# Optimization experiments

Hardware: AMD Instinct MI355X
Metric: run time of the kernel (lower is better)

Reference implementation:

```python
import jax, jax.numpy as jnp
import numpy as np

B, LQ, LK, E, H = 8, 1024, 1024, 512, 8
D = E // H
NEG = -2.0**32 + 1  # padding value used by original torch code


def setup_inputs() -> dict:
    key = jax.random.key(0)
    ks = jax.random.split(key, 6)
    s = 0.02
    return {
        "x1": jax.random.normal(ks[0], (B, LQ, E), jnp.float32),
        "x2": jax.random.normal(ks[1], (B, LK, E), jnp.float32),
        "Wq": jax.random.normal(ks[2], (E, E), jnp.float32) * s,
        "bq": jnp.zeros((E,), jnp.float32),
        "Wk": jax.random.normal(ks[3], (E, E), jnp.float32) * s,
        "bk": jnp.zeros((E,), jnp.float32),
        "Wv": jax.random.normal(ks[4], (E, E), jnp.float32) * s,
        "bv": jnp.zeros((E,), jnp.float32),
    }


def _split_heads(t):
    # torch: cat(split(t, E//H, dim=2), dim=0) -> head-major [H, B, L, D]
    b, l, _ = t.shape
    return jnp.moveaxis(t.reshape(b, l, H, D), 2, 0)


def reference(x1, x2, Wq, bq, Wk, bk, Wv, bv):
    # ReLU-activated projections (nn.Linear: x @ W.T + b)
    q = jax.nn.relu(x1 @ Wq.T + bq)  # [B,LQ,E]
    k = jax.nn.relu(x2 @ Wk.T + bk)  # [B,LK,E]
    v = jax.nn.relu(x2 @ Wv.T + bv)  # [B,LK,E]

    q_, k_, v_ = _split_heads(q), _split_heads(k), _split_heads(v)  # [H,B,L,D]

    # scaled scores; original scales by sqrt(emb_size), not sqrt(d_head)
    scores = jnp.einsum('hbqd,hbkd->hbqk', q_, k_) / jnp.sqrt(jnp.float32(E))

    # sin-based key mask from raw x2
    key_mask = jnp.sin(jnp.abs(jnp.sum(x2, -1)))  # [B,LK]
    scores = jnp.where(key_mask[None, :, None, :] <= 0, NEG, scores)

    attn = jax.nn.softmax(scores, axis=-1)

    # sin-based query mask from raw x1, applied after softmax
    query_mask = jnp.sin(jnp.abs(jnp.sum(x1, -1)))  # [B,LQ]
    attn = attn * query_mask[None, :, :, None]

    out = jnp.einsum('hbqk,hbkd->hbqd', attn, v_)  # [H,B,LQ,D]
    out = jnp.moveaxis(out, 0, 2).reshape(B, LQ, E)  # merge heads back
    return out + q  # residual add with activated query projection
```

## Files before the change

kernel.cpp:

```cpp
#include <hip/hip_runtime.h>
#include <hip/hip_bf16.h>
#include <math.h>

typedef short bf16x8 __attribute__((ext_vector_type(8)));
typedef float f32x4 __attribute__((ext_vector_type(4)));
typedef unsigned int u32;
typedef unsigned short u16;

constexpr int Bb = 8, LQn = 1024, LKn = 1024, En = 512, Hn = 8, Dn = 64;
constexpr int Mtok = Bb * LQn;
constexpr float KCOEF = 0.06376246332977306f;

__device__ __forceinline__ u16 f2bf(float f) {
  u32 u = __builtin_bit_cast(u32, f);
  u32 r = (u + 0x7fffu + ((u >> 16) & 1u)) >> 16;
  return (u16)r;
}
__device__ __forceinline__ float bf2f(u16 h) {
  u32 u = ((u32)h) << 16;
  return __builtin_bit_cast(float, u);
}
__device__ __forceinline__ u16 f2bf_hw(float f) {
  return __builtin_bit_cast(u16, __float2bfloat16(f));
}

__device__ __forceinline__ void async_lds16(const void* gsrc, void* ldst) {
  __builtin_amdgcn_global_load_lds(
      (const __attribute__((address_space(1))) u32*)gsrc,
      (__attribute__((address_space(3))) u32*)ldst, 16, 0, 0);
}

__global__ void prep_kernel(const float* __restrict__ x1, const float* __restrict__ x2,
                            u16* __restrict__ x1b, u16* __restrict__ x2b,
                            float* __restrict__ qmask, float* __restrict__ kbias,
                            const float* __restrict__ Wq, const float* __restrict__ Wk,
                            const float* __restrict__ Wv, u16* __restrict__ wqb,
                            u16* __restrict__ wkb, u16* __restrict__ wvb) {
  int blk = blockIdx.x;
  if (blk < 4096) {
    int id = blk * 4 + (threadIdx.x >> 6);
    int lane = threadIdx.x & 63;
    const float* x; u16* xb; int row; bool isq;
    if (id < Mtok) { x = x1; xb = x1b; row = id; isq = true; }
    else           { x = x2; xb = x2b; row = id - Mtok; isq = false; }
    const float4* p = reinterpret_cast<const float4*>(x + (size_t)row * En);
    ushort4* ob = reinterpret_cast<ushort4*>(xb + (size_t)row * En);
    double s = 0.0;
#pragma unroll
    for (int j = 0; j < En / 256; ++j) {
      float4 v = p[lane + j * 64];
      s += (double)v.x + (double)v.y + (double)v.z + (double)v.w;
      ushort4 o;
      o.x = f2bf(v.x); o.y = f2bf(v.y); o.z = f2bf(v.z); o.w = f2bf(v.w);
      ob[lane + j * 64] = o;
    }
#pragma unroll
    for (int off = 32; off > 0; off >>= 1) s += __shfl_down(s, off, 64);
    if (lane == 0) {
      float sv = (float)sin(fabs(s));
      if (isq) qmask[row] = sv;
      else     kbias[row] = sv > 0.f ? 0.f : -3.0e38f;
    }
  } else {
    int n4 = En * En / 4;
    int j = (blk - 4096) * 256 + threadIdx.x;
    const float* src; u16* dst;
    if (j < n4) { src = Wq; dst = wqb; }
    else if (j < 2 * n4) { src = Wk; dst = wkb; j -= n4; }
    else { src = Wv; dst = wvb; j -= 2 * n4; }
    float4 v = reinterpret_cast<const float4*>(src)[j];
    ushort4 o;
    o.x = f2bf(v.x); o.y = f2bf(v.y); o.z = f2bf(v.z); o.w = f2bf(v.w);
    reinterpret_cast<ushort4*>(dst)[j] = o;
  }
}

template <int BIAS_ROW>
__device__ __forceinline__ void gemm_core(
    const u16* __restrict__ A, const u16* __restrict__ Bm,
    const float* __restrict__ bias, u16* __restrict__ C,
    int ldc, float coef, int row0, int col0) {
  constexpr int K = 512, BK = 64;
  __shared__ u16 sA[2][128 * BK];
  __shared__ u16 sB[2][128 * BK];
  int tid = threadIdx.x;
  int lane = tid & 63;
  int w = tid >> 6;
  int wm = w >> 2, wn = w & 3;
  int rgrp = lane >> 4, cidx = lane & 15;

  f32x4 acc[4][2];
#pragma unroll
  for (int mi = 0; mi < 4; ++mi)
#pragma unroll
    for (int ni = 0; ni < 2; ++ni) acc[mi][ni] = f32x4{0.f, 0.f, 0.f, 0.f};

  auto stage = [&](int kt, int buf) {
    int k0 = kt * BK;
#pragma unroll
    for (int rr = 0; rr < 2; ++rr) {
      int cid = rr * 512 + tid;
      int r = cid >> 3, c = cid & 7;
      int cg = c ^ (r & 7);
      async_lds16(A + (size_t)(row0 + r) * K + k0 + cg * 8, &sA[buf][cid * 8]);
    }
#pragma unroll
    for (int rr = 0; rr < 2; ++rr) {
      int cid = rr * 512 + tid;
      int r = cid >> 3, c = cid & 7;
      int cg = c ^ (r & 7);
      async_lds16(Bm + (size_t)(col0 + r) * K + k0 + cg * 8, &sB[buf][cid * 8]);
    }
  };

  stage(0, 0);
  __syncthreads();

  for (int kt = 0; kt < K / BK; ++kt) {
    int cur = kt & 1;
    if (kt < K / BK - 1) stage(kt + 1, cur ^ 1);
#pragma unroll
    for (int kk = 0; kk < 2; ++kk) {
      bf16x8 a[4], b[2];
#pragma unroll
      for (int mi = 0; mi < 4; ++mi) {
        int row = wm * 64 + mi * 16 + cidx;
        a[mi] = *reinterpret_cast<const bf16x8*>(
            &sA[cur][row * BK + ((kk * 4 + rgrp) ^ (row & 7)) * 8]);
      }
#pragma unroll
      for (int ni = 0; ni < 2; ++ni) {
        int row = wn * 32 + ni * 16 + cidx;
        b[ni] = *reinterpret_cast<const bf16x8*>(
            &sB[cur][row * BK + ((kk * 4 + rgrp) ^ (row & 7)) * 8]);
      }
#pragma unroll
      for (int mi = 0; mi < 4; ++mi)
#pragma unroll
        for (int ni = 0; ni < 2; ++ni)
          acc[mi][ni] = __builtin_amdgcn_mfma_f32_16x16x32_bf16(a[mi], b[ni], acc[mi][ni], 0, 0, 0);
    }
    __syncthreads();
  }
#pragma unroll
  for (int mi = 0; mi < 4; ++mi)
#pragma unroll
    for (int ni = 0; ni < 2; ++ni)
#pragma unroll
      for (int r = 0; r < 4; ++r) {
        int grow = row0 + wm * 64 + mi * 16 + rgrp * 4 + r;
        int gcol = col0 + wn * 32 + ni * 16 + cidx;
        float v = acc[mi][ni][r] + (BIAS_ROW ? bias[grow] : bias[gcol]);
        v = v > 0.f ? v : 0.f;
        C[(size_t)grow * ldc + gcol] = f2bf(v * coef);
      }
}

__global__ __launch_bounds__(512, 4) void gemm3(
    const u16* __restrict__ x1b, const u16* __restrict__ wqb, const float* __restrict__ bq,
    u16* __restrict__ qbq,
    const u16* __restrict__ x2b, const u16* __restrict__ wkb, const float* __restrict__ bk,
    u16* __restrict__ kbk,
    const u16* __restrict__ wvb, const float* __restrict__ bv, u16* __restrict__ vtb) {
  int z = blockIdx.z;
  if (z == 0) {
    gemm_core<0>(x1b, wqb, bq, qbq, En, 1.0f, blockIdx.x * 128, blockIdx.y * 128);
  } else if (z == 1) {
    gemm_core<0>(x2b, wkb, bk, kbk, En, KCOEF, blockIdx.x * 128, blockIdx.y * 128);
  } else {
    gemm_core<1>(wvb, x2b, bv, vtb, Mtok, 1.0f, blockIdx.y * 128, blockIdx.x * 128);
  }
}

__global__ __launch_bounds__(256, 4) void attn_kernel(
    const u16* __restrict__ qb, const u16* __restrict__ kb, const u16* __restrict__ vtb,
    const float* __restrict__ kbias, const float* __restrict__ qmask,
    float* __restrict__ out) {
  __shared__ u16 sK[2][64 * 64];
  __shared__ u16 sV[2][64 * 64];
  __shared__ u16 sQP[64 * 64];
  int tid = threadIdx.x, lane = tid & 63, w = tid >> 6;
  int bh = blockIdx.x, qblk = blockIdx.y;
  int b = bh >> 3, h = bh & 7;
  int rgrp = lane >> 4, cidx = lane & 15;

  const u16* qbase = qb + ((size_t)(b * LQn) + qblk * 64) * En + h * Dn;
  const u16* kbase = kb + (size_t)(b * LKn) * En + h * Dn;
  const u16* vbase = vtb + (size_t)(h * Dn) * Mtok + b * LKn;
  const float* kmb = kbias + b * LKn;

  auto stageKV = [&](int kt, int buf) {
#pragma unroll
    for (int rr = 0; rr < 2; ++rr) {
      int cid = rr * 256 + tid;
      int r = cid >> 3, c = cid & 7;
      int cg = c ^ (r & 7);
      async_lds16(kbase + (size_t)(kt * 64 + r) * En + cg * 8, &sK[buf][cid * 8]);
      async_lds16(vbase + (size_t)r * Mtok + kt * 64 + cg * 8, &sV[buf][cid * 8]);
    }
  };

#pragma unroll
  for (int rr = 0; rr < 2; ++rr) {
    int cid = rr * 256 + tid;
    int r = cid >> 3, c = cid & 7;
    int cg = c ^ (r & 7);
    async_lds16(qbase + (size_t)r * En + cg * 8, &sQP[cid * 8]);
  }
  stageKV(0, 0);
  __syncthreads();

  bf16x8 qa0, qa1;
  {
    int row = w * 16 + cidx;
    qa0 = *reinterpret_cast<const bf16x8*>(&sQP[row * 64 + (rgrp ^ (row & 7)) * 8]);
    qa1 = *reinterpret_cast<const bf16x8*>(&sQP[row * 64 + ((4 + rgrp) ^ (row & 7)) * 8]);
  }

  f32x4 acc_o[4];
#pragma unroll
  for (int dt = 0; dt < 4; ++dt) acc_o[dt] = f32x4{0.f, 0.f, 0.f, 0.f};
  float den = 0.f;

  int prow = w * 16 + cidx;
  char* sPbyte = reinterpret_cast<char*>(sQP);

  for (int kt = 0; kt < LKn / 64; ++kt) {
    int cur = kt & 1;
    if (kt < LKn / 64 - 1) stageKV(kt + 1, cur ^ 1);
#pragma unroll
    for (int ktile = 0; ktile < 4; ++ktile) {
      int krow = ktile * 16 + cidx;
      bf16x8 kf0 = *reinterpret_cast<const bf16x8*>(
          &sK[cur][krow * 64 + (rgrp ^ (krow & 7)) * 8]);
      bf16x8 kf1 = *reinterpret_cast<const bf16x8*>(
          &sK[cur][krow * 64 + ((4 + rgrp) ^ (krow & 7)) * 8]);
      float4 km4 = *reinterpret_cast<const float4*>(&kmb[kt * 64 + ktile * 16 + rgrp * 4]);
      f32x4 s;
      s[0] = km4.x; s[1] = km4.y; s[2] = km4.z; s[3] = km4.w;
      s = __builtin_amdgcn_mfma_f32_16x16x32_bf16(kf0, qa0, s, 0, 0, 0);
      s = __builtin_amdgcn_mfma_f32_16x16x32_bf16(kf1, qa1, s, 0, 0, 0);
      float p0 = __builtin_amdgcn_exp2f(s[0]);
      float p1 = __builtin_amdgcn_exp2f(s[1]);
      float p2 = __builtin_amdgcn_exp2f(s[2]);
      float p3 = __builtin_amdgcn_exp2f(s[3]);
      den += (p0 + p1) + (p2 + p3);
      ushort4 pk;
      pk.x = f2bf_hw(p0); pk.y = f2bf_hw(p1); pk.z = f2bf_hw(p2); pk.w = f2bf_hw(p3);
      int gran = ktile * 2 + (rgrp >> 1);
      int boff = prow * 128 + ((gran ^ (prow & 7)) << 4) + ((rgrp & 1) << 3);
      *reinterpret_cast<ushort4*>(sPbyte + boff) = pk;
    }
    __builtin_amdgcn_s_setprio(1);
#pragma unroll
    for (int kk = 0; kk < 2; ++kk) {
      bf16x8 pa = *reinterpret_cast<const bf16x8*>(
          &sQP[prow * 64 + ((kk * 4 + rgrp) ^ (prow & 7)) * 8]);
#pragma unroll
      for (int dt = 0; dt < 4; ++dt) {
        int vrow = dt * 16 + cidx;
        bf16x8 vf = *reinterpret_cast<const bf16x8*>(
            &sV[cur][vrow * 64 + ((kk * 4 + rgrp) ^ (vrow & 7)) * 8]);
        acc_o[dt] = __builtin_amdgcn_mfma_f32_16x16x32_bf16(pa, vf, acc_o[dt], 0, 0, 0);
      }
    }
    __builtin_amdgcn_s_setprio(0);
    __syncthreads();
  }
  den += __shfl_xor(den, 16, 64);
  den += __shfl_xor(den, 32, 64);

  const float* qmb = qmask + (size_t)b * LQn + qblk * 64 + w * 16;
  const u16* qres = qbase + (size_t)(w * 16) * En;
  float* obase = out + ((size_t)(b * LQn) + qblk * 64 + w * 16) * En + h * Dn;
#pragma unroll
  for (int r = 0; r < 4; ++r) {
    int qr = rgrp * 4 + r;
    float denq = __shfl(den, qr, 64);
    float fac = qmb[qr] / denq;
#pragma unroll
    for (int dt = 0; dt < 4; ++dt) {
      float v = acc_o[dt][r] * fac + bf2f(qres[(size_t)qr * En + dt * 16 + cidx]);
      obase[(size_t)qr * En + dt * 16 + cidx] = v;
    }
  }
}

extern "C" void kernel_launch(void* const* d_in, const int* in_sizes, int n_in,
                              void* d_out, int out_size, void* d_ws, size_t ws_size,
                              hipStream_t stream) {
  const float* x1 = (const float*)d_in[0];
  const float* x2 = (const float*)d_in[1];
  const float* Wq = (const float*)d_in[2];
  const float* bq = (const float*)d_in[3];
  const float* Wk = (const float*)d_in[4];
  const float* bk = (const float*)d_in[5];
  const float* Wv = (const float*)d_in[6];
  const float* bv = (const float*)d_in[7];
  float* out = (float*)d_out;

  char* ws = (char*)d_ws;
  size_t o = 0;
  u16* x1b = (u16*)(ws + o); o += (size_t)Mtok * En * 2;
  u16* x2b = (u16*)(ws + o); o += (size_t)Mtok * En * 2;
  u16* wqb = (u16*)(ws + o); o += (size_t)En * En * 2;
  u16* wkb = (u16*)(ws + o); o += (size_t)En * En * 2;
  u16* wvb = (u16*)(ws + o); o += (size_t)En * En * 2;
  u16* qbq = (u16*)(ws + o); o += (size_t)Mtok * En * 2;
  u16* kbk = (u16*)(ws + o); o += (size_t)Mtok * En * 2;
  u16* vtb = (u16*)(ws + o); o += (size_t)Mtok * En * 2;
  float* kbias = (float*)(ws + o); o += (size_t)Mtok * 4;
  float* qmask = (float*)(ws + o); o += (size_t)Mtok * 4;

  prep_kernel<<<4864, 256, 0, stream>>>(x1, x2, x1b, x2b, qmask, kbias,
                                        Wq, Wk, Wv, wqb, wkb, wvb);

  dim3 g3(Mtok / 128, En / 128, 3);
  gemm3<<<g3, 512, 0, stream>>>(x1b, wqb, bq, qbq, x2b, wkb, bk, kbk, wvb, bv, vtb);

  dim3 ga(Bb * Hn, LQn / 64);
  attn_kernel<<<ga, 256, 0, stream>>>(qbq, kbk, vtb, kbias, qmask, out);
}
```

Baseline: 69.39 us.

## Use 32x32 MFMA attention tiles, keep P in registers, split keys across waves

The attention kernel moves from 16x16x32 to 32x32x16 bf16 MFMA tiles. Each wave now handles 32 queries by 32 keys of every 64-key tile, so the four waves split queries and keys two ways. The probability fragment is rearranged in registers with v_permlane32_swap instead of being written to LDS and read back, which removes an LDS round trip and its bank traffic per tile. In exchange, the two key-half waves must combine their partial outputs and softmax denominators through LDS at the end. The denominator now also sums the bf16-rounded probabilities, so it matches the values fed into the PV product.

```diff
diff --git a/kernel.cpp b/kernel.cpp
--- a/kernel.cpp
+++ b/kernel.cpp
@@ -4,7 +4,9 @@
 
 typedef short bf16x8 __attribute__((ext_vector_type(8)));
 typedef float f32x4 __attribute__((ext_vector_type(4)));
+typedef float f32x16 __attribute__((ext_vector_type(16)));
 typedef unsigned int u32;
+typedef unsigned int u32x4 __attribute__((ext_vector_type(4)));
 typedef unsigned short u16;
 
 constexpr int Bb = 8, LQn = 1024, LKn = 1024, En = 512, Hn = 8, Dn = 64;
@@ -182,7 +184,8 @@
   int tid = threadIdx.x, lane = tid & 63, w = tid >> 6;
   int bh = blockIdx.x, qblk = blockIdx.y;
   int b = bh >> 3, h = bh & 7;
-  int rgrp = lane >> 4, cidx = lane & 15;
+  int l31 = lane & 31, hi = lane >> 5;
+  int qh = w & 1, kh = w >> 1;
 
   const u16* qbase = qb + ((size_t)(b * LQn) + qblk * 64) * En + h * Dn;
   const u16* kbase = kb + (size_t)(b * LKn) * En + h * Dn;
@@ -210,79 +213,107 @@
   stageKV(0, 0);
   __syncthreads();
 
-  bf16x8 qa0, qa1;
+  bf16x8 qf[4];
   {
-    int row = w * 16 + cidx;
-    qa0 = *reinterpret_cast<const bf16x8*>(&sQP[row * 64 + (rgrp ^ (row & 7)) * 8]);
-    qa1 = *reinterpret_cast<const bf16x8*>(&sQP[row * 64 + ((4 + rgrp) ^ (row & 7)) * 8]);
-  }
-
-  f32x4 acc_o[4];
-#pragma unroll
-  for (int dt = 0; dt < 4; ++dt) acc_o[dt] = f32x4{0.f, 0.f, 0.f, 0.f};
+    int qrow = qh * 32 + l31;
+#pragma unroll
+    for (int c = 0; c < 4; ++c) {
+      int chunk = (c * 2 + hi) ^ (qrow & 7);
+      qf[c] = *reinterpret_cast<const bf16x8*>(&sQP[qrow * 64 + chunk * 8]);
+    }
+  }
+
+  f32x16 acc[2];
+  acc[0] = 0.f; acc[1] = 0.f;
   float den = 0.f;
-
-  int prow = w * 16 + cidx;
-  char* sPbyte = reinterpret_cast<char*>(sQP);
 
   for (int kt = 0; kt < LKn / 64; ++kt) {
     int cur = kt & 1;
     if (kt < LKn / 64 - 1) stageKV(kt + 1, cur ^ 1);
-#pragma unroll
-    for (int ktile = 0; ktile < 4; ++ktile) {
-      int krow = ktile * 16 + cidx;
-      bf16x8 kf0 = *reinterpret_cast<const bf16x8*>(
-          &sK[cur][krow * 64 + (rgrp ^ (krow & 7)) * 8]);
-      bf16x8 kf1 = *reinterpret_cast<const bf16x8*>(
-          &sK[cur][krow * 64 + ((4 + rgrp) ^ (krow & 7)) * 8]);
-      float4 km4 = *reinterpret_cast<const float4*>(&kmb[kt * 64 + ktile * 16 + rgrp * 4]);
-      f32x4 s;
-      s[0] = km4.x; s[1] = km4.y; s[2] = km4.z; s[3] = km4.w;
-      s = __builtin_amdgcn_mfma_f32_16x16x32_bf16(kf0, qa0, s, 0, 0, 0);
-      s = __builtin_amdgcn_mfma_f32_16x16x32_bf16(kf1, qa1, s, 0, 0, 0);
-      float p0 = __builtin_amdgcn_exp2f(s[0]);
-      float p1 = __builtin_amdgcn_exp2f(s[1]);
-      float p2 = __builtin_amdgcn_exp2f(s[2]);
-      float p3 = __builtin_amdgcn_exp2f(s[3]);
-      den += (p0 + p1) + (p2 + p3);
-      ushort4 pk;
-      pk.x = f2bf_hw(p0); pk.y = f2bf_hw(p1); pk.z = f2bf_hw(p2); pk.w = f2bf_hw(p3);
-      int gran = ktile * 2 + (rgrp >> 1);
-      int boff = prow * 128 + ((gran ^ (prow & 7)) << 4) + ((rgrp & 1) << 3);
-      *reinterpret_cast<ushort4*>(sPbyte + boff) = pk;
+    bf16x8 kf[4];
+    int krow = kh * 32 + l31;
+    const u16* sKc = sK[cur];
+#pragma unroll
+    for (int c = 0; c < 4; ++c) {
+      int chunk = (c * 2 + hi) ^ (krow & 7);
+      kf[c] = *reinterpret_cast<const bf16x8*>(&sKc[krow * 64 + chunk * 8]);
+    }
+    f32x16 s;
+#pragma unroll
+    for (int j = 0; j < 4; ++j) {
+      float4 kb4 = *reinterpret_cast<const float4*>(&kmb[kt * 64 + kh * 32 + 8 * j + 4 * hi]);
+      s[4 * j + 0] = kb4.x; s[4 * j + 1] = kb4.y;
+      s[4 * j + 2] = kb4.z; s[4 * j + 3] = kb4.w;
+    }
+#pragma unroll
+    for (int c = 0; c < 4; ++c)
+      s = __builtin_amdgcn_mfma_f32_32x32x16_bf16(kf[c], qf[c], s, 0, 0, 0);
+    u32 pw[8];
+#pragma unroll
+    for (int m = 0; m < 8; ++m) {
+      float p0 = __builtin_amdgcn_exp2f(s[2 * m]);
+      float p1 = __builtin_amdgcn_exp2f(s[2 * m + 1]);
+      u16 b0 = f2bf_hw(p0), b1 = f2bf_hw(p1);
+      den += bf2f(b0) + bf2f(b1);
+      pw[m] = (u32)b0 | ((u32)b1 << 16);
+    }
+    bf16x8 paf[2];
+#pragma unroll
+    for (int kc = 0; kc < 2; ++kc) {
+      u32 a0 = pw[4 * kc + 0], a2 = pw[4 * kc + 2];
+      u32 a1 = pw[4 * kc + 1], a3 = pw[4 * kc + 3];
+      asm volatile("v_permlane32_swap_b32 %0, %1" : "+v"(a0), "+v"(a2));
+      asm volatile("v_permlane32_swap_b32 %0, %1" : "+v"(a1), "+v"(a3));
+      u32x4 t; t[0] = a0; t[1] = a1; t[2] = a2; t[3] = a3;
+      paf[kc] = __builtin_bit_cast(bf16x8, t);
     }
     __builtin_amdgcn_s_setprio(1);
-#pragma unroll
-    for (int kk = 0; kk < 2; ++kk) {
-      bf16x8 pa = *reinterpret_cast<const bf16x8*>(
-          &sQP[prow * 64 + ((kk * 4 + rgrp) ^ (prow & 7)) * 8]);
-#pragma unroll
-      for (int dt = 0; dt < 4; ++dt) {
-        int vrow = dt * 16 + cidx;
-        bf16x8 vf = *reinterpret_cast<const bf16x8*>(
-            &sV[cur][vrow * 64 + ((kk * 4 + rgrp) ^ (vrow & 7)) * 8]);
-        acc_o[dt] = __builtin_amdgcn_mfma_f32_16x16x32_bf16(pa, vf, acc_o[dt], 0, 0, 0);
+    const u16* sVc = sV[cur];
+#pragma unroll
+    for (int dt = 0; dt < 2; ++dt) {
+      int vrow = dt * 32 + l31;
+#pragma unroll
+      for (int kc = 0; kc < 2; ++kc) {
+        int chunk = (kh * 4 + kc * 2 + hi) ^ (vrow & 7);
+        bf16x8 vf = *reinterpret_cast<const bf16x8*>(&sVc[vrow * 64 + chunk * 8]);
+        acc[dt] = __builtin_amdgcn_mfma_f32_32x32x16_bf16(paf[kc], vf, acc[dt], 0, 0, 0);
       }
     }
     __builtin_amdgcn_s_setprio(0);
     __syncthreads();
   }
-  den += __shfl_xor(den, 16, 64);
   den += __shfl_xor(den, 32, 64);
 
-  const float* qmb = qmask + (size_t)b * LQn + qblk * 64 + w * 16;
-  const u16* qres = qbase + (size_t)(w * 16) * En;
-  float* obase = out + ((size_t)(b * LQn) + qblk * 64 + w * 16) * En + h * Dn;
-#pragma unroll
-  for (int r = 0; r < 4; ++r) {
-    int qr = rgrp * 4 + r;
-    float denq = __shfl(den, qr, 64);
-    float fac = qmb[qr] / denq;
-#pragma unroll
-    for (int dt = 0; dt < 4; ++dt) {
-      float v = acc_o[dt][r] * fac + bf2f(qres[(size_t)qr * En + dt * 16 + cidx]);
-      obase[(size_t)qr * En + dt * 16 + cidx] = v;
-    }
+  float* dslab = (float*)sV;
+  if (kh == 1) {
+    float* aslab = (w == 2) ? (float*)sQP : (float*)sK;
+#pragma unroll
+    for (int dt = 0; dt < 2; ++dt)
+#pragma unroll
+      for (int rg = 0; rg < 16; ++rg)
+        aslab[(dt * 16 + rg) * 64 + lane] = acc[dt][rg];
+    if (lane < 32) dslab[qh * 32 + l31] = den;
+  }
+  __syncthreads();
+  if (kh == 0) {
+    float* pslab = (w == 0) ? (float*)sQP : (float*)sK;
+    float denf = den + dslab[qh * 32 + l31];
+    if (lane < 32) dslab[64 + qh * 32 + l31] = denf;
+    const float* qmb = qmask + (size_t)b * LQn + qblk * 64 + qh * 32;
+    const u16* qres = qbase + (size_t)(qh * 32) * En;
+    float* obase = out + ((size_t)(b * LQn) + qblk * 64 + qh * 32) * En + h * Dn;
+#pragma unroll
+    for (int dt = 0; dt < 2; ++dt)
+#pragma unroll
+      for (int rg = 0; rg < 16; ++rg) {
+        int q = (rg & 3) + 8 * (rg >> 2) + 4 * hi;
+        float a = acc[dt][rg] + pslab[(dt * 16 + rg) * 64 + lane];
+        float denq = dslab[64 + qh * 32 + q];
+        float fac = qmb[q] / denq;
+        int d = dt * 32 + l31;
+        float v = a * fac + bf2f(qres[(size_t)q * En + d]);
+        obase[(size_t)q * En + d] = v;
+      }
   }
 }
 
```

After: 80.12 us. 15.5% more time.
